# Kernel tuning notes

Measured on AMD Instinct MI355X. Metric: run time of the kernel, lower is better.

Reference implementation:

```python
import jax, jax.numpy as jnp
import numpy as np
import math

B, C, H, W = 4, 256, 64, 64
DQK = max(1, C // 8)  # 32


def setup_inputs() -> dict:
    key = jax.random.key(0)
    ks = jax.random.split(key, 6)
    x = jax.random.normal(ks[0], (B, C, H, W), dtype=jnp.float32)
    Wq = jax.random.normal(ks[1], (DQK, C), dtype=jnp.float32) * (1.0 / math.sqrt(C))
    bq = jnp.zeros((DQK,), dtype=jnp.float32)
    Wk = jax.random.normal(ks[2], (DQK, C), dtype=jnp.float32) * (1.0 / math.sqrt(C))
    bk = jnp.zeros((DQK,), dtype=jnp.float32)
    Wv = jax.random.normal(ks[3], (C, C), dtype=jnp.float32) * (1.0 / math.sqrt(C))
    bv = jnp.zeros((C,), dtype=jnp.float32)
    gamma = jax.random.normal(ks[4], (1,), dtype=jnp.float32)
    return {"x": x, "Wq": Wq, "bq": bq, "Wk": Wk, "bk": bk, "Wv": Wv, "bv": bv, "gamma": gamma}


def reference(x, Wq, bq, Wk, bk, Wv, bv, gamma):
    b, c, h, w = x.shape
    n = h * w
    xf = x.reshape(b, c, n)                                  # [B, C, N]
    # 1x1 convs == per-pixel linear projections
    q = jnp.einsum('bcn,dc->bdn', xf, Wq) + bq[None, :, None]  # [B, DQK, N]
    k = jnp.einsum('bcn,dc->bdn', xf, Wk) + bk[None, :, None]  # [B, DQK, N]
    v = jnp.einsum('bcn,oc->bon', xf, Wv) + bv[None, :, None]  # [B, C, N]
    scale = 1.0 / math.sqrt(q.shape[1] + 1e-8)
    attn = jnp.einsum('bdi,bdj->bij', q, k) * scale            # [B, N, N]
    attn = jax.nn.softmax(attn, axis=-1)
    out = jnp.einsum('bcj,bij->bci', v, attn)                  # [B, C, N]
    out = out.reshape(b, c, h, w)
    return gamma[0] * out + x
```

## Files before the change

### kernel.cpp

```cpp
#include <hip/hip_runtime.h>
#include <hip/hip_bf16.h>
#include <math.h>

#define BB   4
#define CC   256
#define DQK  32
#define NN   4096
#define QBLK 64
#define KVB  128
#define NQB  (NN / QBLK)
#define NTILES (NN / KVB)
#define SCALE 0.17677669529663687f
#define LOG2E 1.4426950408889634f

typedef short  bf16x8 __attribute__((ext_vector_type(8)));
typedef float  f32x4  __attribute__((ext_vector_type(4)));
typedef unsigned short u16;
typedef unsigned int   u32;

__device__ __forceinline__ u16 f2bf(float f) {
    __hip_bfloat16 h = __float2bfloat16(f);
    return *reinterpret_cast<u16*>(&h);
}

__device__ __forceinline__ u32 pack2bf(float a, float b) {
    const u32 ua = __builtin_bit_cast(u32, a) + 0x8000u;
    const u32 ub = __builtin_bit_cast(u32, b) + 0x8000u;
    return (ua >> 16) | (ub & 0xFFFF0000u);
}

__global__ __launch_bounds__(256) void wprep_kernel(
    const float* __restrict__ Wq, const float* __restrict__ bq,
    const float* __restrict__ Wk, const float* __restrict__ bk,
    const float* __restrict__ Wv, const float* __restrict__ bv,
    u16* __restrict__ Wb, float* __restrict__ biasb)
{
    const int r = blockIdx.x;
    const int t = threadIdx.x;
    float w, bias;
    if (r < DQK)          { w = Wq[r * CC + t] * (SCALE * LOG2E); bias = bq[r] * (SCALE * LOG2E); }
    else if (r < 2 * DQK) { w = Wk[(r - DQK) * CC + t];           bias = bk[r - DQK];  }
    else                  { w = Wv[(r - 2 * DQK) * CC + t];       bias = bv[r - 2 * DQK]; }
    Wb[r * CC + t] = f2bf(w);
    if (t == 0) biasb[r] = bias;
}

__global__ __launch_bounds__(512) void qkv_gemm(
    const float* __restrict__ x,
    const u16* __restrict__ Wb, const float* __restrict__ biasb,
    u16* __restrict__ qt, u16* __restrict__ kt, u16* __restrict__ v)
{
    __shared__ __align__(16) u16 xT[64][256];

    const int b   = blockIdx.y;
    const int n0  = blockIdx.x * 64;
    const int t   = threadIdx.x;

    {
        const int n_l = t & 63;
        const int cg  = t >> 6;
        const int sw  = (n_l & 15) << 3;
        #pragma unroll
        for (int p = 0; p < 8; ++p) {
            const int c0 = p * 32 + cg * 4;
            const float f0 = x[((size_t)b * CC + c0 + 0) * NN + n0 + n_l];
            const float f1 = x[((size_t)b * CC + c0 + 1) * NN + n0 + n_l];
            const float f2 = x[((size_t)b * CC + c0 + 2) * NN + n0 + n_l];
            const float f3 = x[((size_t)b * CC + c0 + 3) * NN + n0 + n_l];
            uint2 pk;
            pk.x = pack2bf(f0, f1);
            pk.y = pack2bf(f2, f3);
            *(uint2*)&xT[n_l][c0 ^ sw] = pk;
        }
    }
    __syncthreads();

    const int wid = t >> 6;
    const int mw  = wid & 3;
    const int nw  = wid >> 2;
    const int lane = t & 63;
    const int g    = lane >> 4;
    const int c16  = lane & 15;

    f32x4 acc[5][2];
    #pragma unroll
    for (int mf = 0; mf < 5; ++mf)
        #pragma unroll
        for (int nf = 0; nf < 2; ++nf)
            #pragma unroll
            for (int r = 0; r < 4; ++r) acc[mf][nf][r] = 0.f;

    const int rsw = c16 << 3;

    #pragma unroll
    for (int kk = 0; kk < 8; ++kk) {
        bf16x8 xf[2];
        #pragma unroll
        for (int nf = 0; nf < 2; ++nf)
            xf[nf] = *(const bf16x8*)&xT[nw * 32 + nf * 16 + c16][(kk * 32 + g * 8) ^ rsw];
        #pragma unroll
        for (int mf = 0; mf < 5; ++mf) {
            const bf16x8 wf = *(const bf16x8*)(Wb + (size_t)(mw * 80 + mf * 16 + c16) * CC + kk * 32 + g * 8);
            #pragma unroll
            for (int nf = 0; nf < 2; ++nf)
                acc[mf][nf] = __builtin_amdgcn_mfma_f32_16x16x32_bf16(wf, xf[nf], acc[mf][nf], 0, 0, 0);
        }
    }

    #pragma unroll
    for (int mf = 0; mf < 5; ++mf) {
        #pragma unroll
        for (int nf = 0; nf < 2; ++nf) {
            const int n = n0 + nw * 32 + nf * 16 + c16;
            #pragma unroll
            for (int r = 0; r < 4; ++r) {
                const int row = mw * 80 + mf * 16 + g * 4 + r;
                const float val = acc[mf][nf][r] + biasb[row];
                if (row < DQK)
                    qt[((size_t)b * NN + n) * DQK + row] = f2bf(val);
                else if (row < 2 * DQK)
                    kt[((size_t)b * NN + n) * DQK + (row - DQK)] = f2bf(val);
                else
                    v[((size_t)b * CC + (row - 2 * DQK)) * NN + n] = f2bf(val);
            }
        }
    }
}

__global__ __launch_bounds__(512, 2) void attn_kernel(
    const u16* __restrict__ qt, const u16* __restrict__ kt,
    const u16* __restrict__ vg,
    const float* __restrict__ x, const float* __restrict__ gamma_p,
    float* __restrict__ out)
{
    const int id   = blockIdx.x;
    const int xcd  = id & 7;
    const int b    = xcd >> 1;
    const int i0   = (((xcd & 1) << 5) + (id >> 3)) * QBLK;
    const int t    = threadIdx.x;
    const int wid  = t >> 6;
    const int lane = t & 63;
    const int g    = lane >> 4;
    const int c16  = lane & 15;
    const int jh   = wid >> 2;
    const int mw   = wid & 3;

    __shared__ __align__(16) u16 P_s[2][QBLK * KVB];
    __shared__ float l_s[2][QBLK];

    const u16* ktb = kt + (size_t)b * NN * DQK;
    const u16* vb  = vg + (size_t)b * CC * NN + (size_t)(wid * 32) * NN;

    const bf16x8 qa = *(const bf16x8*)(qt + ((size_t)b * NN + i0 + mw * 16 + c16) * DQK + g * 8);

    bf16x8 kb[4];
    #pragma unroll
    for (int jf = 0; jf < 4; ++jf)
        kb[jf] = *(const bf16x8*)(ktb + (size_t)(jh * 64 + jf * 16 + c16) * DQK + g * 8);

    f32x4 accv[2][4];
    #pragma unroll
    for (int cf = 0; cf < 2; ++cf)
        #pragma unroll
        for (int qf = 0; qf < 4; ++qf)
            #pragma unroll
            for (int r = 0; r < 4; ++r) accv[cf][qf][r] = 0.f;

    float l_acc = 0.f;

    const int rowbase = (mw * 16 + c16) * KVB;
    const int swz     = c16 << 3;

    for (int jt = 0; jt < NTILES; ++jt) {
        const int j0  = jt * KVB;
        const int buf = jt & 1;

        bf16x8 va[2][4];
        #pragma unroll
        for (int cf = 0; cf < 2; ++cf)
            #pragma unroll
            for (int ksl = 0; ksl < 4; ++ksl)
                va[cf][ksl] = *(const bf16x8*)(vb + (size_t)(cf * 16 + c16) * NN + j0 + ksl * 32 + g * 8);

        f32x4 sres[4];
        #pragma unroll
        for (int jf = 0; jf < 4; ++jf)
            sres[jf] = __builtin_amdgcn_mfma_f32_16x16x32_bf16(kb[jf], qa, (f32x4){0.f, 0.f, 0.f, 0.f}, 0, 0, 0);

        #pragma unroll
        for (int jf = 0; jf < 4; ++jf) {
            const float p0 = __builtin_amdgcn_exp2f(sres[jf][0]);
            const float p1 = __builtin_amdgcn_exp2f(sres[jf][1]);
            const float p2 = __builtin_amdgcn_exp2f(sres[jf][2]);
            const float p3 = __builtin_amdgcn_exp2f(sres[jf][3]);
            l_acc += (p0 + p1) + (p2 + p3);
            uint2 pk;
            pk.x = pack2bf(p0, p1);
            pk.y = pack2bf(p2, p3);
            *(uint2*)&P_s[buf][rowbase + ((jh * 64 + jf * 16 + g * 4) ^ swz)] = pk;
        }

        asm volatile("s_waitcnt lgkmcnt(0)" ::: "memory");
        __builtin_amdgcn_s_barrier();
        __builtin_amdgcn_sched_barrier(0);

        const int jn = ((jt + 1) & (NTILES - 1)) * KVB;
        #pragma unroll
        for (int jf = 0; jf < 4; ++jf)
            kb[jf] = *(const bf16x8*)(ktb + (size_t)(jn + jh * 64 + jf * 16 + c16) * DQK + g * 8);

        __builtin_amdgcn_s_setprio(1);
        #pragma unroll
        for (int ksl = 0; ksl < 4; ++ksl) {
            #pragma unroll
            for (int qf = 0; qf < 4; ++qf) {
                const int row = c16 + 16 * qf;
                const int e   = (row * KVB + ksl * 32 + g * 8) ^ ((row & 15) << 3);
                const bf16x8 pb = *(const bf16x8*)&P_s[buf][e];
                #pragma unroll
                for (int cf = 0; cf < 2; ++cf)
                    accv[cf][qf] = __builtin_amdgcn_mfma_f32_16x16x32_bf16(va[cf][ksl], pb, accv[cf][qf], 0, 0, 0);
            }
        }
        __builtin_amdgcn_s_setprio(0);
    }

    l_acc += __shfl_xor(l_acc, 16);
    l_acc += __shfl_xor(l_acc, 32);
    if (lane < 16) l_s[jh][mw * 16 + c16] = l_acc;
    __syncthreads();

    const float gam = gamma_p[0];
    #pragma unroll
    for (int qf = 0; qf < 4; ++qf) {
        const int   qloc = c16 + 16 * qf;
        const int   qcol = i0 + qloc;
        const float linv = 1.0f / (l_s[0][qloc] + l_s[1][qloc]);
        #pragma unroll
        for (int cf = 0; cf < 2; ++cf) {
            #pragma unroll
            for (int r = 0; r < 4; ++r) {
                const int    c = wid * 32 + cf * 16 + g * 4 + r;
                const size_t o = ((size_t)b * CC + c) * NN + qcol;
                out[o] = gam * (accv[cf][qf][r] * linv) + x[o];
            }
        }
    }
}

extern "C" void kernel_launch(void* const* d_in, const int* in_sizes, int n_in,
                              void* d_out, int out_size, void* d_ws, size_t ws_size,
                              hipStream_t stream)
{
    const float* x     = (const float*)d_in[0];
    const float* Wq    = (const float*)d_in[1];
    const float* bq    = (const float*)d_in[2];
    const float* Wk    = (const float*)d_in[3];
    const float* bk    = (const float*)d_in[4];
    const float* Wv    = (const float*)d_in[5];
    const float* bv    = (const float*)d_in[6];
    const float* gamma = (const float*)d_in[7];
    float* out = (float*)d_out;

    u16* qt   = (u16*)d_ws;
    u16* kt   = qt + (size_t)BB * NN * DQK;
    u16* v    = kt + (size_t)BB * NN * DQK;
    u16* Wb   = v  + (size_t)BB * CC * NN;
    float* biasb = (float*)(Wb + 320 * CC);

    wprep_kernel<<<dim3(320), 256, 0, stream>>>(Wq, bq, Wk, bk, Wv, bv, Wb, biasb);
    qkv_gemm<<<dim3(NN / 64, BB), 512, 0, stream>>>(x, Wb, biasb, qt, kt, v);
    attn_kernel<<<dim3(BB * NQB), 512, 0, stream>>>(qt, kt, v, x, gamma, out);
}
```

Baseline: 104.7 us.

## Repartition attention waves to own full key tiles and drop block barriers

Each wave now computes scores for its 16 queries over the whole 128-key tile and keeps the resulting P in its own private LDS slice. This removes the per-tile block-wide barrier and the cross-wave softmax-sum exchange. Each wave then covers 128 output channels instead of 32, and V fragments are double-buffered across the four k-slices so loads overlap the MFMAs. The cost is redundant work: the two waves sharing a query group recompute the same QK scores and exps. Register pressure also rises (8 kb, 16 V fragments, 8 accumulators), and every V tile is loaded by four waves.

After: 283.8 us. +171.2%, slower.

```diff
diff --git a/kernel.cpp b/kernel.cpp
--- a/kernel.cpp
+++ b/kernel.cpp
@@ -142,53 +142,53 @@
     const int lane = t & 63;
     const int g    = lane >> 4;
     const int c16  = lane & 15;
-    const int jh   = wid >> 2;
     const int mw   = wid & 3;
-
-    __shared__ __align__(16) u16 P_s[2][QBLK * KVB];
-    __shared__ float l_s[2][QBLK];
+    const int ch   = wid >> 2;
+
+    __shared__ __align__(16) u16 P_s[8][16 * KVB];
 
     const u16* ktb = kt + (size_t)b * NN * DQK;
-    const u16* vb  = vg + (size_t)b * CC * NN + (size_t)(wid * 32) * NN;
+    const u16* vb  = vg + (size_t)b * CC * NN + (size_t)(ch * 128) * NN;
+    u16* const Pw  = &P_s[wid][0];
 
     const bf16x8 qa = *(const bf16x8*)(qt + ((size_t)b * NN + i0 + mw * 16 + c16) * DQK + g * 8);
 
-    bf16x8 kb[4];
-    #pragma unroll
-    for (int jf = 0; jf < 4; ++jf)
-        kb[jf] = *(const bf16x8*)(ktb + (size_t)(jh * 64 + jf * 16 + c16) * DQK + g * 8);
-
-    f32x4 accv[2][4];
-    #pragma unroll
-    for (int cf = 0; cf < 2; ++cf)
-        #pragma unroll
-        for (int qf = 0; qf < 4; ++qf)
-            #pragma unroll
-            for (int r = 0; r < 4; ++r) accv[cf][qf][r] = 0.f;
+    bf16x8 kb[8];
+    #pragma unroll
+    for (int jf = 0; jf < 8; ++jf)
+        kb[jf] = *(const bf16x8*)(ktb + (size_t)(jf * 16 + c16) * DQK + g * 8);
+
+    f32x4 acc[8];
+    #pragma unroll
+    for (int cf = 0; cf < 8; ++cf)
+        #pragma unroll
+        for (int r = 0; r < 4; ++r) acc[cf][r] = 0.f;
 
     float l_acc = 0.f;
 
-    const int rowbase = (mw * 16 + c16) * KVB;
-    const int swz     = c16 << 3;
+    const int swz   = (c16 & 7) << 3;
+    const int wrow  = c16 * KVB;
+
+    bf16x8 vaA[8], vaB[8];
 
     for (int jt = 0; jt < NTILES; ++jt) {
-        const int j0  = jt * KVB;
-        const int buf = jt & 1;
-
-        bf16x8 va[2][4];
-        #pragma unroll
-        for (int cf = 0; cf < 2; ++cf)
-            #pragma unroll
-            for (int ksl = 0; ksl < 4; ++ksl)
-                va[cf][ksl] = *(const bf16x8*)(vb + (size_t)(cf * 16 + c16) * NN + j0 + ksl * 32 + g * 8);
-
-        f32x4 sres[4];
-        #pragma unroll
-        for (int jf = 0; jf < 4; ++jf)
+        const int j0 = jt * KVB;
+
+        f32x4 sres[8];
+        #pragma unroll
+        for (int jf = 0; jf < 8; ++jf)
             sres[jf] = __builtin_amdgcn_mfma_f32_16x16x32_bf16(kb[jf], qa, (f32x4){0.f, 0.f, 0.f, 0.f}, 0, 0, 0);
 
-        #pragma unroll
-        for (int jf = 0; jf < 4; ++jf) {
+        const int jn = ((jt + 1) & (NTILES - 1)) * KVB;
+        #pragma unroll
+        for (int jf = 0; jf < 8; ++jf)
+            kb[jf] = *(const bf16x8*)(ktb + (size_t)(jn + jf * 16 + c16) * DQK + g * 8);
+        #pragma unroll
+        for (int cf = 0; cf < 8; ++cf)
+            vaA[cf] = *(const bf16x8*)(vb + (size_t)(cf * 16 + c16) * NN + j0 + 0 * 32 + g * 8);
+
+        #pragma unroll
+        for (int jf = 0; jf < 8; ++jf) {
             const float p0 = __builtin_amdgcn_exp2f(sres[jf][0]);
             const float p1 = __builtin_amdgcn_exp2f(sres[jf][1]);
             const float p2 = __builtin_amdgcn_exp2f(sres[jf][2]);
@@ -197,53 +197,43 @@
             uint2 pk;
             pk.x = pack2bf(p0, p1);
             pk.y = pack2bf(p2, p3);
-            *(uint2*)&P_s[buf][rowbase + ((jh * 64 + jf * 16 + g * 4) ^ swz)] = pk;
-        }
-
-        asm volatile("s_waitcnt lgkmcnt(0)" ::: "memory");
-        __builtin_amdgcn_s_barrier();
-        __builtin_amdgcn_sched_barrier(0);
-
-        const int jn = ((jt + 1) & (NTILES - 1)) * KVB;
-        #pragma unroll
-        for (int jf = 0; jf < 4; ++jf)
-            kb[jf] = *(const bf16x8*)(ktb + (size_t)(jn + jh * 64 + jf * 16 + c16) * DQK + g * 8);
-
-        __builtin_amdgcn_s_setprio(1);
-        #pragma unroll
-        for (int ksl = 0; ksl < 4; ++ksl) {
-            #pragma unroll
-            for (int qf = 0; qf < 4; ++qf) {
-                const int row = c16 + 16 * qf;
-                const int e   = (row * KVB + ksl * 32 + g * 8) ^ ((row & 15) << 3);
-                const bf16x8 pb = *(const bf16x8*)&P_s[buf][e];
-                #pragma unroll
-                for (int cf = 0; cf < 2; ++cf)
-                    accv[cf][qf] = __builtin_amdgcn_mfma_f32_16x16x32_bf16(va[cf][ksl], pb, accv[cf][qf], 0, 0, 0);
-            }
-        }
-        __builtin_amdgcn_s_setprio(0);
+            *(uint2*)&Pw[wrow + ((jf * 16 + g * 4) ^ swz)] = pk;
+        }
+
+#define PV_STEP(KS, VC, VN, PRE)                                                          \
+        {                                                                                 \
+            if (PRE) {                                                                    \
+                _Pragma("unroll")                                                         \
+                for (int cf = 0; cf < 8; ++cf)                                            \
+                    VN[cf] = *(const bf16x8*)(vb + (size_t)(cf * 16 + c16) * NN + j0 + ((KS) + 1) * 32 + g * 8); \
+            }                                                                             \
+            const bf16x8 pb = *(const bf16x8*)&Pw[wrow + (((KS) * 32 + g * 8) ^ swz)];    \
+            __builtin_amdgcn_s_setprio(1);                                                \
+            _Pragma("unroll")                                                             \
+            for (int cf = 0; cf < 8; ++cf)                                                \
+                acc[cf] = __builtin_amdgcn_mfma_f32_16x16x32_bf16(VC[cf], pb, acc[cf], 0, 0, 0); \
+            __builtin_amdgcn_s_setprio(0);                                                \
+        }
+        PV_STEP(0, vaA, vaB, 1)
+        PV_STEP(1, vaB, vaA, 1)
+        PV_STEP(2, vaA, vaB, 1)
+        PV_STEP(3, vaB, vaA, 0)
+#undef PV_STEP
     }
 
     l_acc += __shfl_xor(l_acc, 16);
     l_acc += __shfl_xor(l_acc, 32);
-    if (lane < 16) l_s[jh][mw * 16 + c16] = l_acc;
-    __syncthreads();
-
-    const float gam = gamma_p[0];
-    #pragma unroll
-    for (int qf = 0; qf < 4; ++qf) {
-        const int   qloc = c16 + 16 * qf;
-        const int   qcol = i0 + qloc;
-        const float linv = 1.0f / (l_s[0][qloc] + l_s[1][qloc]);
-        #pragma unroll
-        for (int cf = 0; cf < 2; ++cf) {
-            #pragma unroll
-            for (int r = 0; r < 4; ++r) {
-                const int    c = wid * 32 + cf * 16 + g * 4 + r;
-                const size_t o = ((size_t)b * CC + c) * NN + qcol;
-                out[o] = gam * (accv[cf][qf][r] * linv) + x[o];
-            }
+
+    const float gam  = gamma_p[0];
+    const float linv = 1.0f / l_acc;
+    const int   qcol = i0 + mw * 16 + c16;
+    #pragma unroll
+    for (int cf = 0; cf < 8; ++cf) {
+        #pragma unroll
+        for (int r = 0; r < 4; ++r) {
+            const int    c = ch * 128 + cf * 16 + g * 4 + r;
+            const size_t o = ((size_t)b * CC + c) * NN + qcol;
+            out[o] = gam * (acc[cf][r] * linv) + x[o];
         }
     }
 }
```
